# Kernel tuning notes

Hardware: AMD Instinct MI355X
Metric: run time of the kernel (lower is better)

The kernel has to match this reference:

```python
import jax, jax.numpy as jnp
import numpy as np

TOP_K = 4


def setup_inputs() -> dict:
    key = jax.random.key(0)
    ks = jax.random.split(key, 9)
    B, T, D, H, NE = 2, 1024, 2048, 1408, 16
    s = 0.02
    return {
        "x": jax.random.normal(ks[0], (B, T, D), jnp.float32),
        "gate_w": jax.random.normal(ks[1], (NE, D), jnp.float32) * s,
        "gate_b": jax.random.normal(ks[2], (NE,), jnp.float32) * s,
        "w1_shared": jax.random.normal(ks[3], (D, H), jnp.float32) * s,
        "w2_shared": jax.random.normal(ks[4], (H, D), jnp.float32) * s,
        "w3_shared": jax.random.normal(ks[5], (D, H), jnp.float32) * s,
        "w1_routed": jax.random.normal(ks[6], (NE, D, H), jnp.float32) * s,
        "w2_routed": jax.random.normal(ks[7], (NE, H, D), jnp.float32) * s,
        "w3_routed": jax.random.normal(ks[8], (NE, D, H), jnp.float32) * s,
    }


def reference(x, gate_w, gate_b, w1_shared, w2_shared, w3_shared,
              w1_routed, w2_routed, w3_routed):
    n_experts = w1_routed.shape[0]
    # --- gate (IGate): sigmoid scores + bias, top-k, renormalize ---
    logits = jnp.einsum('ed,btd->bte', gate_w, x)            # [B,T,NE]
    scores = jax.nn.sigmoid(logits) + gate_b
    weights, indices = jax.lax.top_k(scores, TOP_K)          # [B,T,K]
    weights = weights / weights.sum(-1, keepdims=True)
    # --- shared experts: standard SwiGLU ---
    shared_out = (jax.nn.silu(x @ w1_shared) * (x @ w3_shared)) @ w2_shared
    # --- routed experts: dense compute-all then mask with router probs ---
    one_hot = jax.nn.one_hot(indices, n_experts, dtype=x.dtype)   # [B,T,K,NE]
    router_probs = (weights[..., None] * one_hot).sum(-2)         # [B,T,NE]
    h1 = jnp.einsum('btd,edc->btec', x, w1_routed)                # [B,T,NE,H]
    h2 = jnp.einsum('btd,edc->btec', x, w3_routed)
    h3 = jax.nn.silu(h1 * h2)                                     # NOTE: silu of product, as in source
    experts_out = jnp.einsum('btec,ecd->bted', h3, w2_routed)     # [B,T,NE,D]
    routed_out = jnp.einsum('bted,bte->btd', experts_out, router_probs)
    return shared_out + routed_out
```

## Files before the change

### kernel.cpp

```cpp
#include <hip/hip_runtime.h>

typedef unsigned short u16;
typedef short s16x8 __attribute__((ext_vector_type(8)));
typedef float f32x4 __attribute__((ext_vector_type(4)));

#define NTOK 2048
#define DDIM 2048
#define HDIM 1408
#define CAP  2048
#define SLOT ((size_t)DDIM * (size_t)HDIM)

#define OFF_XB   ((size_t)0)
#define OFF_W1T  ((size_t)8388608)
#define OFF_W3T  (OFF_W1T + (size_t)17*SLOT*2)
#define OFF_W2T  (OFF_W3T + (size_t)17*SLOT*2)
#define OFF_H3   (OFF_W2T + (size_t)17*SLOT*2)
#define OFF_TOK  (OFF_H3 + (size_t)17*CAP*HDIM*2)
#define OFF_WT   (OFF_TOK + (size_t)17*CAP*4)
#define OFF_CNT  (OFF_WT + (size_t)17*CAP*4)

__device__ __forceinline__ u16 f2bf(float f) {
  unsigned u = __float_as_uint(f);
  u += 0x7fffu + ((u >> 16) & 1u);
  return (u16)(u >> 16);
}

__device__ __forceinline__ int imin(int a, int b) { return a < b ? a : b; }

__device__ __forceinline__ void async_cp16(const void* g, void* l) {
  __builtin_amdgcn_global_load_lds(
      (const __attribute__((address_space(1))) unsigned int*)g,
      (__attribute__((address_space(3))) unsigned int*)l, 16, 0, 0);
}

__global__ __launch_bounds__(256) void cvt_x(const float* __restrict__ src,
                                             u16* __restrict__ dst, int n4) {
  int i = blockIdx.x * 256 + threadIdx.x;
  if (i >= n4) return;
  float4 v = ((const float4*)src)[i];
  ushort4 o;
  o.x = f2bf(v.x); o.y = f2bf(v.y); o.z = f2bf(v.z); o.w = f2bf(v.w);
  ((ushort4*)dst)[i] = o;
}

__global__ __launch_bounds__(256) void transpose_cvt(const float* __restrict__ src,
                                                     u16* __restrict__ dst,
                                                     int R, int C) {
  __shared__ float tile[64][65];
  size_t slice = (size_t)blockIdx.z * (size_t)R * (size_t)C;
  src += slice; dst += slice;
  int r0 = blockIdx.y * 64, c0 = blockIdx.x * 64;
  int tid = threadIdx.x;
  for (int s = tid; s < 1024; s += 256) {
    int row = s >> 4;
    int c4 = (s & 15) << 2;
    float4 v = *(const float4*)(src + (size_t)(r0 + row) * C + c0 + c4);
    tile[row][c4] = v.x; tile[row][c4 + 1] = v.y;
    tile[row][c4 + 2] = v.z; tile[row][c4 + 3] = v.w;
  }
  __syncthreads();
  for (int s = tid; s < 1024; s += 256) {
    int crow = s >> 4;
    int r4 = (s & 15) << 2;
    ushort4 o;
    o.x = f2bf(tile[r4 + 0][crow]);
    o.y = f2bf(tile[r4 + 1][crow]);
    o.z = f2bf(tile[r4 + 2][crow]);
    o.w = f2bf(tile[r4 + 3][crow]);
    *(ushort4*)(dst + (size_t)(c0 + crow) * R + r0 + r4) = o;
  }
}

__global__ __launch_bounds__(256) void gate_kernel(const float* __restrict__ x,
                                                   const float* __restrict__ gw,
                                                   const float* __restrict__ gb,
                                                   int* __restrict__ tok,
                                                   float* __restrict__ wt,
                                                   int* __restrict__ counts) {
  int t = blockIdx.x;
  __shared__ float lsX[DDIM];
  __shared__ float lsLogit[16];
  int tid = threadIdx.x;
  const float4* xr = (const float4*)(x + (size_t)t * DDIM);
  for (int s = tid; s < DDIM / 4; s += 256) {
    float4 v = xr[s];
    lsX[s * 4 + 0] = v.x; lsX[s * 4 + 1] = v.y;
    lsX[s * 4 + 2] = v.z; lsX[s * 4 + 3] = v.w;
  }
  if (tid == 17) { tok[16 * CAP + t] = t; wt[16 * CAP + t] = 1.0f; }
  __syncthreads();
  int e = tid >> 4, sub = tid & 15;
  const float* gwe = gw + (size_t)e * DDIM;
  float p = 0.f;
  for (int d = sub; d < DDIM; d += 16) p += lsX[d] * gwe[d];
  p += __shfl_xor(p, 8, 16);
  p += __shfl_xor(p, 4, 16);
  p += __shfl_xor(p, 2, 16);
  p += __shfl_xor(p, 1, 16);
  if (sub == 0) lsLogit[e] = p;
  __syncthreads();
  if (tid == 0) {
    float s[16];
    for (int i = 0; i < 16; i++) s[i] = 1.f / (1.f + expf(-lsLogit[i])) + gb[i];
    unsigned used = 0;
    int sel[4]; float sw[4]; float sum = 0.f;
    for (int k = 0; k < 4; k++) {
      int bi = -1; float bv = -1e30f;
      for (int i = 0; i < 16; i++)
        if (!((used >> i) & 1u) && s[i] > bv) { bv = s[i]; bi = i; }
      used |= 1u << bi; sel[k] = bi; sw[k] = bv; sum += bv;
    }
    float inv = 1.f / sum;
    for (int k = 0; k < 4; k++) {
      int pos = atomicAdd(&counts[sel[k]], 1);
      tok[sel[k] * CAP + pos] = t;
      wt[sel[k] * CAP + pos] = sw[k] * inv;
    }
  }
}

__global__ __launch_bounds__(256) void gemm1(const u16* __restrict__ xb,
                                             const u16* __restrict__ w1t,
                                             const u16* __restrict__ w3t,
                                             const int* __restrict__ tok,
                                             const int* __restrict__ counts,
                                             u16* __restrict__ h3) {
  int e = blockIdx.z;
  int cnt = (e == 16) ? NTOK : counts[e];
  int m0 = blockIdx.y * 128;
  if (m0 >= cnt) return;
  int n0 = blockIdx.x * 128;
  const u16* B1 = w1t + (size_t)e * SLOT;
  const u16* B3 = w3t + (size_t)e * SLOT;

  __shared__ alignas(16) u16 lsA[128 * 32];
  __shared__ alignas(16) u16 lsB1[128 * 32];
  __shared__ alignas(16) u16 lsB3[128 * 32];

  int tid = threadIdx.x, w = tid >> 6, lane = tid & 63;
  int lrow = lane >> 2;
  int lcolb = (lane & 3) * 16;
  int ra0 = w * 32 + lrow, ra1 = w * 32 + 16 + lrow;
  int t0 = tok[e * CAP + imin(m0 + ra0, cnt - 1)];
  int t1 = tok[e * CAP + imin(m0 + ra1, cnt - 1)];
  const char* gA0 = (const char*)(xb + (size_t)t0 * DDIM) + lcolb;
  const char* gA1 = (const char*)(xb + (size_t)t1 * DDIM) + lcolb;
  const char* gB1a = (const char*)(B1 + (size_t)(n0 + ra0) * DDIM) + lcolb;
  const char* gB1b = (const char*)(B1 + (size_t)(n0 + ra1) * DDIM) + lcolb;
  const char* gB3a = (const char*)(B3 + (size_t)(n0 + ra0) * DDIM) + lcolb;
  const char* gB3b = (const char*)(B3 + (size_t)(n0 + ra1) * DDIM) + lcolb;
  u16* dA0 = lsA + (w * 32) * 32;      u16* dA1 = lsA + (w * 32 + 16) * 32;
  u16* dB1a = lsB1 + (w * 32) * 32;    u16* dB1b = lsB1 + (w * 32 + 16) * 32;
  u16* dB3a = lsB3 + (w * 32) * 32;    u16* dB3b = lsB3 + (w * 32 + 16) * 32;

  f32x4 acc1[4][4] = {}; f32x4 acc3[4][4] = {};
  int lr = lane & 15, quad = lane >> 4;
  int wm = (w >> 1) * 64, wn = (w & 1) * 64;

  for (int kk = 0; kk < DDIM / 32; ++kk) {
    async_cp16(gA0, dA0);  async_cp16(gA1, dA1);
    async_cp16(gB1a, dB1a); async_cp16(gB1b, dB1b);
    async_cp16(gB3a, dB3a); async_cp16(gB3b, dB3b);
    gA0 += 64; gA1 += 64; gB1a += 64; gB1b += 64; gB3a += 64; gB3b += 64;
    __syncthreads();
    s16x8 af[4], b1f[4], b3f[4];
#pragma unroll
    for (int i = 0; i < 4; ++i)
      af[i] = *(const s16x8*)(lsA + (wm + i * 16 + lr) * 32 + quad * 8);
#pragma unroll
    for (int j = 0; j < 4; ++j) {
      b1f[j] = *(const s16x8*)(lsB1 + (wn + j * 16 + lr) * 32 + quad * 8);
      b3f[j] = *(const s16x8*)(lsB3 + (wn + j * 16 + lr) * 32 + quad * 8);
    }
#pragma unroll
    for (int i = 0; i < 4; ++i)
#pragma unroll
      for (int j = 0; j < 4; ++j) {
        acc1[i][j] = __builtin_amdgcn_mfma_f32_16x16x32_bf16(af[i], b1f[j], acc1[i][j], 0, 0, 0);
        acc3[i][j] = __builtin_amdgcn_mfma_f32_16x16x32_bf16(af[i], b3f[j], acc3[i][j], 0, 0, 0);
      }
    __syncthreads();
  }

  bool routed = (e < 16);
  size_t hbase = (size_t)e * CAP;
#pragma unroll
  for (int i = 0; i < 4; ++i) {
#pragma unroll
    for (int r = 0; r < 4; ++r) {
      int rl = wm + i * 16 + quad * 4 + r;
      int grow = m0 + rl;
      if (grow >= cnt) continue;
      u16* orow = h3 + (hbase + grow) * HDIM + n0 + wn + lr;
#pragma unroll
      for (int j = 0; j < 4; ++j) {
        float c1 = acc1[i][j][r], c3 = acc3[i][j][r];
        float hv;
        if (routed) { float z = c1 * c3; hv = z / (1.f + __expf(-z)); }
        else        { hv = c1 / (1.f + __expf(-c1)) * c3; }
        orow[j * 16] = f2bf(hv);
      }
    }
  }
}

__global__ __launch_bounds__(256) void gemm2(const u16* __restrict__ h3,
                                             const u16* __restrict__ w2t,
                                             const int* __restrict__ tok,
                                             const float* __restrict__ wt,
                                             const int* __restrict__ counts,
                                             float* __restrict__ out) {
  int e = blockIdx.z;
  int cnt = (e == 16) ? NTOK : counts[e];
  int m0 = blockIdx.y * 128;
  if (m0 >= cnt) return;
  int n0 = blockIdx.x * 128;
  const u16* B = w2t + (size_t)e * SLOT;

  __shared__ alignas(16) u16 lsA[128 * 32];
  __shared__ alignas(16) u16 lsB[128 * 32];
  __shared__ int lsTok[128];
  __shared__ float lsWt[128];

  int tid = threadIdx.x, w = tid >> 6, lane = tid & 63;
  if (tid < 128) {
    int idx = imin(m0 + tid, cnt - 1);
    lsTok[tid] = tok[e * CAP + idx];
    lsWt[tid] = wt[e * CAP + idx];
  }
  int lrow = lane >> 2;
  int lcolb = (lane & 3) * 16;
  int ra0 = w * 32 + lrow, ra1 = w * 32 + 16 + lrow;
  size_t hbase = (size_t)e * CAP;
  const char* gA0 = (const char*)(h3 + (hbase + imin(m0 + ra0, cnt - 1)) * HDIM) + lcolb;
  const char* gA1 = (const char*)(h3 + (hbase + imin(m0 + ra1, cnt - 1)) * HDIM) + lcolb;
  const char* gB0 = (const char*)(B + (size_t)(n0 + ra0) * HDIM) + lcolb;
  const char* gB1 = (const char*)(B + (size_t)(n0 + ra1) * HDIM) + lcolb;
  u16* dA0 = lsA + (w * 32) * 32;  u16* dA1 = lsA + (w * 32 + 16) * 32;
  u16* dB0 = lsB + (w * 32) * 32;  u16* dB1 = lsB + (w * 32 + 16) * 32;

  f32x4 acc[4][4] = {};
  int lr = lane & 15, quad = lane >> 4;
  int wm = (w >> 1) * 64, wn = (w & 1) * 64;

  for (int kk = 0; kk < HDIM / 32; ++kk) {
    async_cp16(gA0, dA0); async_cp16(gA1, dA1);
    async_cp16(gB0, dB0); async_cp16(gB1, dB1);
    gA0 += 64; gA1 += 64; gB0 += 64; gB1 += 64;
    __syncthreads();
    s16x8 af[4], bf[4];
#pragma unroll
    for (int i = 0; i < 4; ++i)
      af[i] = *(const s16x8*)(lsA + (wm + i * 16 + lr) * 32 + quad * 8);
#pragma unroll
    for (int j = 0; j < 4; ++j)
      bf[j] = *(const s16x8*)(lsB + (wn + j * 16 + lr) * 32 + quad * 8);
#pragma unroll
    for (int i = 0; i < 4; ++i)
#pragma unroll
      for (int j = 0; j < 4; ++j)
        acc[i][j] = __builtin_amdgcn_mfma_f32_16x16x32_bf16(af[i], bf[j], acc[i][j], 0, 0, 0);
    __syncthreads();
  }

#pragma unroll
  for (int i = 0; i < 4; ++i) {
#pragma unroll
    for (int r = 0; r < 4; ++r) {
      int rl = wm + i * 16 + quad * 4 + r;
      int grow = m0 + rl;
      if (grow >= cnt) continue;
      float wgt = lsWt[rl];
      float* orow = out + (size_t)lsTok[rl] * DDIM + n0 + wn + lr;
#pragma unroll
      for (int j = 0; j < 4; ++j)
        atomicAdd(orow + j * 16, acc[i][j][r] * wgt);
    }
  }
}

extern "C" void kernel_launch(void* const* d_in, const int* in_sizes, int n_in,
                              void* d_out, int out_size, void* d_ws, size_t ws_size,
                              hipStream_t stream) {
  const float* x      = (const float*)d_in[0];
  const float* gate_w = (const float*)d_in[1];
  const float* gate_b = (const float*)d_in[2];
  const float* w1s    = (const float*)d_in[3];
  const float* w2s    = (const float*)d_in[4];
  const float* w3s    = (const float*)d_in[5];
  const float* w1r    = (const float*)d_in[6];
  const float* w2r    = (const float*)d_in[7];
  const float* w3r    = (const float*)d_in[8];
  float* out = (float*)d_out;
  char* ws = (char*)d_ws;

  u16*   xb   = (u16*)(ws + OFF_XB);
  u16*   w1t  = (u16*)(ws + OFF_W1T);
  u16*   w3t  = (u16*)(ws + OFF_W3T);
  u16*   w2t  = (u16*)(ws + OFF_W2T);
  u16*   h3   = (u16*)(ws + OFF_H3);
  int*   tokl = (int*)(ws + OFF_TOK);
  float* wtl  = (float*)(ws + OFF_WT);
  int*   cnts = (int*)(ws + OFF_CNT);

  hipMemsetAsync(out, 0, (size_t)NTOK * DDIM * sizeof(float), stream);
  hipMemsetAsync(cnts, 0, 64, stream);

  cvt_x<<<(NTOK * DDIM / 4 + 255) / 256, 256, 0, stream>>>(x, xb, NTOK * DDIM / 4);

  transpose_cvt<<<dim3(HDIM / 64, DDIM / 64, 16), 256, 0, stream>>>(w1r, w1t, DDIM, HDIM);
  transpose_cvt<<<dim3(HDIM / 64, DDIM / 64, 16), 256, 0, stream>>>(w3r, w3t, DDIM, HDIM);
  transpose_cvt<<<dim3(DDIM / 64, HDIM / 64, 16), 256, 0, stream>>>(w2r, w2t, HDIM, DDIM);
  transpose_cvt<<<dim3(HDIM / 64, DDIM / 64, 1), 256, 0, stream>>>(w1s, w1t + 16 * SLOT, DDIM, HDIM);
  transpose_cvt<<<dim3(HDIM / 64, DDIM / 64, 1), 256, 0, stream>>>(w3s, w3t + 16 * SLOT, DDIM, HDIM);
  transpose_cvt<<<dim3(DDIM / 64, HDIM / 64, 1), 256, 0, stream>>>(w2s, w2t + 16 * SLOT, HDIM, DDIM);

  gate_kernel<<<NTOK, 256, 0, stream>>>(x, gate_w, gate_b, tokl, wtl, cnts);

  gemm1<<<dim3(HDIM / 128, NTOK / 128, 17), 256, 0, stream>>>(xb, w1t, w3t, tokl, cnts, h3);
  gemm2<<<dim3(DDIM / 128, NTOK / 128, 17), 256, 0, stream>>>(h3, w2t, tokl, wtl, cnts, out);
}
```

Measured before the change: 1.184 ms.

## Replace atomic scatter with bf16 expert outputs plus gather-reduce, shrink GEMM N-tile

gemm2 no longer scatters weighted results into the fp32 output with atomicAdd. It writes each expert's weighted rows as bf16 into a workspace buffer that reuses the w1t region, and a new reduce_out kernel gathers the shared row plus the four routed rows per token via an index table recorded by the gate. Both GEMMs drop from 128x128 to 128x64 tiles, swap grid axes so M runs fastest, and request 3 blocks per CU for occupancy. The output memset goes away. The cost is an extra write-and-read pass over a large intermediate, plus bf16 rounding of per-expert partial outputs before summation.

```diff
diff --git a/kernel.cpp b/kernel.cpp
--- a/kernel.cpp
+++ b/kernel.cpp
@@ -2,6 +2,7 @@
 
 typedef unsigned short u16;
 typedef short s16x8 __attribute__((ext_vector_type(8)));
+typedef u16 u16x8 __attribute__((ext_vector_type(8)));
 typedef float f32x4 __attribute__((ext_vector_type(4)));
 
 #define NTOK 2048
@@ -18,13 +19,17 @@
 #define OFF_TOK  (OFF_H3 + (size_t)17*CAP*HDIM*2)
 #define OFF_WT   (OFF_TOK + (size_t)17*CAP*4)
 #define OFF_CNT  (OFF_WT + (size_t)17*CAP*4)
+#define OFF_IDX4 (OFF_CNT + (size_t)256)
+#define OFF_EOUT OFF_W1T
 
 __device__ __forceinline__ u16 f2bf(float f) {
   unsigned u = __float_as_uint(f);
   u += 0x7fffu + ((u >> 16) & 1u);
   return (u16)(u >> 16);
 }
-
+__device__ __forceinline__ float bf2f(u16 v) {
+  return __uint_as_float(((unsigned)v) << 16);
+}
 __device__ __forceinline__ int imin(int a, int b) { return a < b ? a : b; }
 
 __device__ __forceinline__ void async_cp16(const void* g, void* l) {
@@ -76,7 +81,8 @@
                                                    const float* __restrict__ gb,
                                                    int* __restrict__ tok,
                                                    float* __restrict__ wt,
-                                                   int* __restrict__ counts) {
+                                                   int* __restrict__ counts,
+                                                   int* __restrict__ idx4) {
   int t = blockIdx.x;
   __shared__ float lsX[DDIM];
   __shared__ float lsLogit[16];
@@ -115,67 +121,65 @@
       int pos = atomicAdd(&counts[sel[k]], 1);
       tok[sel[k] * CAP + pos] = t;
       wt[sel[k] * CAP + pos] = sw[k] * inv;
-    }
-  }
-}
-
-__global__ __launch_bounds__(256) void gemm1(const u16* __restrict__ xb,
-                                             const u16* __restrict__ w1t,
-                                             const u16* __restrict__ w3t,
-                                             const int* __restrict__ tok,
-                                             const int* __restrict__ counts,
-                                             u16* __restrict__ h3) {
+      idx4[t * 4 + k] = sel[k] * CAP + pos;
+    }
+  }
+}
+
+__global__ __launch_bounds__(256, 3) void gemm1(const u16* __restrict__ xb,
+                                                const u16* __restrict__ w1t,
+                                                const u16* __restrict__ w3t,
+                                                const int* __restrict__ tok,
+                                                const int* __restrict__ counts,
+                                                u16* __restrict__ h3) {
   int e = blockIdx.z;
   int cnt = (e == 16) ? NTOK : counts[e];
-  int m0 = blockIdx.y * 128;
+  int m0 = blockIdx.x * 128;
   if (m0 >= cnt) return;
-  int n0 = blockIdx.x * 128;
+  int n0 = blockIdx.y * 64;
   const u16* B1 = w1t + (size_t)e * SLOT;
   const u16* B3 = w3t + (size_t)e * SLOT;
 
   __shared__ alignas(16) u16 lsA[128 * 32];
-  __shared__ alignas(16) u16 lsB1[128 * 32];
-  __shared__ alignas(16) u16 lsB3[128 * 32];
+  __shared__ alignas(16) u16 lsB1[64 * 32];
+  __shared__ alignas(16) u16 lsB3[64 * 32];
 
   int tid = threadIdx.x, w = tid >> 6, lane = tid & 63;
   int lrow = lane >> 2;
   int lcolb = (lane & 3) * 16;
-  int ra0 = w * 32 + lrow, ra1 = w * 32 + 16 + lrow;
+  int ra0 = w * 32 + lrow, ra1 = ra0 + 16;
   int t0 = tok[e * CAP + imin(m0 + ra0, cnt - 1)];
   int t1 = tok[e * CAP + imin(m0 + ra1, cnt - 1)];
   const char* gA0 = (const char*)(xb + (size_t)t0 * DDIM) + lcolb;
   const char* gA1 = (const char*)(xb + (size_t)t1 * DDIM) + lcolb;
-  const char* gB1a = (const char*)(B1 + (size_t)(n0 + ra0) * DDIM) + lcolb;
-  const char* gB1b = (const char*)(B1 + (size_t)(n0 + ra1) * DDIM) + lcolb;
-  const char* gB3a = (const char*)(B3 + (size_t)(n0 + ra0) * DDIM) + lcolb;
-  const char* gB3b = (const char*)(B3 + (size_t)(n0 + ra1) * DDIM) + lcolb;
-  u16* dA0 = lsA + (w * 32) * 32;      u16* dA1 = lsA + (w * 32 + 16) * 32;
-  u16* dB1a = lsB1 + (w * 32) * 32;    u16* dB1b = lsB1 + (w * 32 + 16) * 32;
-  u16* dB3a = lsB3 + (w * 32) * 32;    u16* dB3b = lsB3 + (w * 32 + 16) * 32;
-
-  f32x4 acc1[4][4] = {}; f32x4 acc3[4][4] = {};
+  const char* gB1 = (const char*)(B1 + (size_t)(n0 + w * 16 + lrow) * DDIM) + lcolb;
+  const char* gB3 = (const char*)(B3 + (size_t)(n0 + w * 16 + lrow) * DDIM) + lcolb;
+  u16* dA0 = lsA + (w * 32) * 32;  u16* dA1 = lsA + (w * 32 + 16) * 32;
+  u16* dB1 = lsB1 + (w * 16) * 32;
+  u16* dB3 = lsB3 + (w * 16) * 32;
+
+  f32x4 acc1[4][2] = {}; f32x4 acc3[4][2] = {};
   int lr = lane & 15, quad = lane >> 4;
-  int wm = (w >> 1) * 64, wn = (w & 1) * 64;
+  int wm = (w >> 1) * 64, wn = (w & 1) * 32;
 
   for (int kk = 0; kk < DDIM / 32; ++kk) {
-    async_cp16(gA0, dA0);  async_cp16(gA1, dA1);
-    async_cp16(gB1a, dB1a); async_cp16(gB1b, dB1b);
-    async_cp16(gB3a, dB3a); async_cp16(gB3b, dB3b);
-    gA0 += 64; gA1 += 64; gB1a += 64; gB1b += 64; gB3a += 64; gB3b += 64;
+    async_cp16(gA0, dA0); async_cp16(gA1, dA1);
+    async_cp16(gB1, dB1); async_cp16(gB3, dB3);
+    gA0 += 64; gA1 += 64; gB1 += 64; gB3 += 64;
     __syncthreads();
-    s16x8 af[4], b1f[4], b3f[4];
+    s16x8 af[4], b1f[2], b3f[2];
 #pragma unroll
     for (int i = 0; i < 4; ++i)
       af[i] = *(const s16x8*)(lsA + (wm + i * 16 + lr) * 32 + quad * 8);
 #pragma unroll
-    for (int j = 0; j < 4; ++j) {
+    for (int j = 0; j < 2; ++j) {
       b1f[j] = *(const s16x8*)(lsB1 + (wn + j * 16 + lr) * 32 + quad * 8);
       b3f[j] = *(const s16x8*)(lsB3 + (wn + j * 16 + lr) * 32 + quad * 8);
     }
 #pragma unroll
     for (int i = 0; i < 4; ++i)
 #pragma unroll
-      for (int j = 0; j < 4; ++j) {
+      for (int j = 0; j < 2; ++j) {
         acc1[i][j] = __builtin_amdgcn_mfma_f32_16x16x32_bf16(af[i], b1f[j], acc1[i][j], 0, 0, 0);
         acc3[i][j] = __builtin_amdgcn_mfma_f32_16x16x32_bf16(af[i], b3f[j], acc3[i][j], 0, 0, 0);
       }
@@ -193,7 +197,7 @@
       if (grow >= cnt) continue;
       u16* orow = h3 + (hbase + grow) * HDIM + n0 + wn + lr;
 #pragma unroll
-      for (int j = 0; j < 4; ++j) {
+      for (int j = 0; j < 2; ++j) {
         float c1 = acc1[i][j][r], c3 = acc3[i][j][r];
         float hv;
         if (routed) { float z = c1 * c3; hv = z / (1.f + __expf(-z)); }
@@ -204,61 +208,54 @@
   }
 }
 
-__global__ __launch_bounds__(256) void gemm2(const u16* __restrict__ h3,
-                                             const u16* __restrict__ w2t,
-                                             const int* __restrict__ tok,
-                                             const float* __restrict__ wt,
-                                             const int* __restrict__ counts,
-                                             float* __restrict__ out) {
+__global__ __launch_bounds__(256, 3) void gemm2(const u16* __restrict__ h3,
+                                                const u16* __restrict__ w2t,
+                                                const int* __restrict__ tok,
+                                                const float* __restrict__ wt,
+                                                const int* __restrict__ counts,
+                                                u16* __restrict__ eout) {
   int e = blockIdx.z;
   int cnt = (e == 16) ? NTOK : counts[e];
-  int m0 = blockIdx.y * 128;
+  int m0 = blockIdx.x * 128;
   if (m0 >= cnt) return;
-  int n0 = blockIdx.x * 128;
+  int n0 = blockIdx.y * 64;
   const u16* B = w2t + (size_t)e * SLOT;
 
   __shared__ alignas(16) u16 lsA[128 * 32];
-  __shared__ alignas(16) u16 lsB[128 * 32];
-  __shared__ int lsTok[128];
+  __shared__ alignas(16) u16 lsB[64 * 32];
   __shared__ float lsWt[128];
 
   int tid = threadIdx.x, w = tid >> 6, lane = tid & 63;
-  if (tid < 128) {
-    int idx = imin(m0 + tid, cnt - 1);
-    lsTok[tid] = tok[e * CAP + idx];
-    lsWt[tid] = wt[e * CAP + idx];
-  }
+  if (tid < 128) lsWt[tid] = wt[e * CAP + imin(m0 + tid, cnt - 1)];
   int lrow = lane >> 2;
   int lcolb = (lane & 3) * 16;
-  int ra0 = w * 32 + lrow, ra1 = w * 32 + 16 + lrow;
+  int ra0 = w * 32 + lrow, ra1 = ra0 + 16;
   size_t hbase = (size_t)e * CAP;
   const char* gA0 = (const char*)(h3 + (hbase + imin(m0 + ra0, cnt - 1)) * HDIM) + lcolb;
   const char* gA1 = (const char*)(h3 + (hbase + imin(m0 + ra1, cnt - 1)) * HDIM) + lcolb;
-  const char* gB0 = (const char*)(B + (size_t)(n0 + ra0) * HDIM) + lcolb;
-  const char* gB1 = (const char*)(B + (size_t)(n0 + ra1) * HDIM) + lcolb;
+  const char* gB  = (const char*)(B + (size_t)(n0 + w * 16 + lrow) * HDIM) + lcolb;
   u16* dA0 = lsA + (w * 32) * 32;  u16* dA1 = lsA + (w * 32 + 16) * 32;
-  u16* dB0 = lsB + (w * 32) * 32;  u16* dB1 = lsB + (w * 32 + 16) * 32;
-
-  f32x4 acc[4][4] = {};
+  u16* dB  = lsB + (w * 16) * 32;
+
+  f32x4 acc[4][2] = {};
   int lr = lane & 15, quad = lane >> 4;
-  int wm = (w >> 1) * 64, wn = (w & 1) * 64;
+  int wm = (w >> 1) * 64, wn = (w & 1) * 32;
 
   for (int kk = 0; kk < HDIM / 32; ++kk) {
-    async_cp16(gA0, dA0); async_cp16(gA1, dA1);
-    async_cp16(gB0, dB0); async_cp16(gB1, dB1);
-    gA0 += 64; gA1 += 64; gB0 += 64; gB1 += 64;
+    async_cp16(gA0, dA0); async_cp16(gA1, dA1); async_cp16(gB, dB);
+    gA0 += 64; gA1 += 64; gB += 64;
     __syncthreads();
-    s16x8 af[4], bf[4];
+    s16x8 af[4], bf[2];
 #pragma unroll
     for (int i = 0; i < 4; ++i)
       af[i] = *(const s16x8*)(lsA + (wm + i * 16 + lr) * 32 + quad * 8);
 #pragma unroll
-    for (int j = 0; j < 4; ++j)
+    for (int j = 0; j < 2; ++j)
       bf[j] = *(const s16x8*)(lsB + (wn + j * 16 + lr) * 32 + quad * 8);
 #pragma unroll
     for (int i = 0; i < 4; ++i)
 #pragma unroll
-      for (int j = 0; j < 4; ++j)
+      for (int j = 0; j < 2; ++j)
         acc[i][j] = __builtin_amdgcn_mfma_f32_16x16x32_bf16(af[i], bf[j], acc[i][j], 0, 0, 0);
     __syncthreads();
   }
@@ -271,12 +268,36 @@
       int grow = m0 + rl;
       if (grow >= cnt) continue;
       float wgt = lsWt[rl];
-      float* orow = out + (size_t)lsTok[rl] * DDIM + n0 + wn + lr;
-#pragma unroll
-      for (int j = 0; j < 4; ++j)
-        atomicAdd(orow + j * 16, acc[i][j][r] * wgt);
-    }
-  }
+      u16* orow = eout + ((size_t)e * CAP + grow) * DDIM + n0 + wn + lr;
+#pragma unroll
+      for (int j = 0; j < 2; ++j)
+        orow[j * 16] = f2bf(acc[i][j][r] * wgt);
+    }
+  }
+}
+
+__global__ __launch_bounds__(256) void reduce_out(const u16* __restrict__ eout,
+                                                  const int* __restrict__ idx4,
+                                                  float* __restrict__ out) {
+  int t = blockIdx.x;
+  int d = threadIdx.x * 8;
+  int i0 = idx4[t * 4 + 0], i1 = idx4[t * 4 + 1];
+  int i2 = idx4[t * 4 + 2], i3 = idx4[t * 4 + 3];
+  u16x8 vs = *(const u16x8*)(eout + ((size_t)(16 * CAP) + t) * DDIM + d);
+  u16x8 v0 = *(const u16x8*)(eout + (size_t)i0 * DDIM + d);
+  u16x8 v1 = *(const u16x8*)(eout + (size_t)i1 * DDIM + d);
+  u16x8 v2 = *(const u16x8*)(eout + (size_t)i2 * DDIM + d);
+  u16x8 v3 = *(const u16x8*)(eout + (size_t)i3 * DDIM + d);
+  float4 o0, o1;
+  float* o = (float*)&o0;
+#pragma unroll
+  for (int k = 0; k < 8; ++k) {
+    float s = bf2f(vs[k]) + bf2f(v0[k]) + bf2f(v1[k]) + bf2f(v2[k]) + bf2f(v3[k]);
+    if (k < 4) ((float*)&o0)[k] = s; else ((float*)&o1)[k - 4] = s;
+  }
+  (void)o;
+  float4* orow = (float4*)(out + (size_t)t * DDIM + d);
+  orow[0] = o0; orow[1] = o1;
 }
 
 extern "C" void kernel_launch(void* const* d_in, const int* in_sizes, int n_in,
@@ -302,8 +323,9 @@
   int*   tokl = (int*)(ws + OFF_TOK);
   float* wtl  = (float*)(ws + OFF_WT);
   int*   cnts = (int*)(ws + OFF_CNT);
-
-  hipMemsetAsync(out, 0, (size_t)NTOK * DDIM * sizeof(float), stream);
+  int*   idx4 = (int*)(ws + OFF_IDX4);
+  u16*   eout = (u16*)(ws + OFF_EOUT);
+
   hipMemsetAsync(cnts, 0, 64, stream);
 
   cvt_x<<<(NTOK * DDIM / 4 + 255) / 256, 256, 0, stream>>>(x, xb, NTOK * DDIM / 4);
@@ -315,8 +337,9 @@
   transpose_cvt<<<dim3(HDIM / 64, DDIM / 64, 1), 256, 0, stream>>>(w3s, w3t + 16 * SLOT, DDIM, HDIM);
   transpose_cvt<<<dim3(DDIM / 64, HDIM / 64, 1), 256, 0, stream>>>(w2s, w2t + 16 * SLOT, HDIM, DDIM);
 
-  gate_kernel<<<NTOK, 256, 0, stream>>>(x, gate_w, gate_b, tokl, wtl, cnts);
-
-  gemm1<<<dim3(HDIM / 128, NTOK / 128, 17), 256, 0, stream>>>(xb, w1t, w3t, tokl, cnts, h3);
-  gemm2<<<dim3(DDIM / 128, NTOK / 128, 17), 256, 0, stream>>>(h3, w2t, tokl, wtl, cnts, out);
-}
+  gate_kernel<<<NTOK, 256, 0, stream>>>(x, gate_w, gate_b, tokl, wtl, cnts, idx4);
+
+  gemm1<<<dim3(NTOK / 128, HDIM / 64, 17), 256, 0, stream>>>(xb, w1t, w3t, tokl, cnts, h3);
+  gemm2<<<dim3(NTOK / 128, DDIM / 64, 17), 256, 0, stream>>>(h3, w2t, tokl, wtl, cnts, eout);
+  reduce_out<<<NTOK, 256, 0, stream>>>(eout, idx4, out);
+}
```

Result: slower. 1.478 ms (+24.8%).
